# Performance work log

Hardware: AMD Instinct MI355X
Metric: run time of the kernel (lower is better)

Reference implementation:

```python
import jax, jax.numpy as jnp
import numpy as np

D = 128; H = 8; L = 3; FF = 512; HID = 512
B = 512; N = 20
KD = D // H
CLIP = 10.0


def _bn(x, g, b):
    # BatchNorm1d over flattened (B*n, D), training-mode batch stats, affine
    m = jnp.mean(x, axis=(0, 1)); v = jnp.var(x, axis=(0, 1))
    return (x - m) * jax.lax.rsqrt(v + 1e-5) * g + b


def _mha(x, Wq, Wk, Wv, Wo):
    q = jnp.einsum('bnd,hdk->hbnk', x, Wq)
    k = jnp.einsum('bnd,hdk->hbnk', x, Wk)
    v = jnp.einsum('bnd,hdk->hbnk', x, Wv)
    a = jax.nn.softmax(jnp.einsum('hbnk,hbmk->hbnm', q, k) / np.float32(np.sqrt(KD)), axis=-1)
    h = jnp.einsum('hbnm,hbmk->hbnk', a, v)
    return jnp.einsum('hbnk,hkd->bnd', h, Wo)


def _encode(x, Wq, Wk, Wv, Wo, g1, b1, fW1, fb1, fW2, fb2, g2, b2):
    for l in range(L):
        x = _bn(x + _mha(x, Wq[l], Wk[l], Wv[l], Wo[l]), g1[l], b1[l])
        f = jnp.maximum(x @ fW1[l] + fb1[l], 0.0) @ fW2[l] + fb2[l]
        x = _bn(x + f, g2[l], b2[l])
    return x


def _forward(coords, Wi, bi, W_ph, enc_Wq, enc_Wk, enc_Wv, enc_Wo, enc_g1, enc_b1,
             enc_ffW1, enc_ffb1, enc_ffW2, enc_ffb2, enc_g2, enc_b2,
             W_node, W_fixed, W_step, W_out, Wc1, bc1, Wc2, bc2):
    Bs, Ns, _ = coords.shape
    bid = jnp.arange(Bs)
    x = coords @ Wi + bi                                   # (B,N,D) initial embeddings
    crd = coords
    node_idx = jnp.broadcast_to(jnp.arange(Ns)[None, :], (Bs, Ns))
    # state is re-made each step, so step context is always the placeholder
    step_ctx = jnp.broadcast_to(W_ph[None, :], (Bs, 2 * D))
    ctx_q = step_ctx @ W_step                              # (B,D), constant across steps
    log_ps = []; irs = []; vals = []; tours = []
    first = prev = cur = None
    for i in range(Ns):  # sequential decode loop (shapes shrink each step)
        n = Ns - i
        E = _encode(x, enc_Wq, enc_Wk, enc_Wv, enc_Wo, enc_g1, enc_b1,
                    enc_ffW1, enc_ffb1, enc_ffW2, enc_ffb2, enc_g2, enc_b2)  # (B,n,D)
        g_mean = jnp.mean(E, axis=1)                       # (B,D)
        q = g_mean @ W_fixed + ctx_q                       # (B,D)
        gK, gV, lK = jnp.split(E @ W_node, 3, axis=-1)     # each (B,n,D)
        qh = q.reshape(Bs, H, KD)
        a = jax.nn.softmax(jnp.einsum('bhk,bnhk->bhn', qh, gK.reshape(Bs, n, H, KD)) / np.float32(np.sqrt(KD)), axis=-1)
        glimpse = jnp.einsum('bhn,bnhk->bhk', a, gV.reshape(Bs, n, H, KD)).reshape(Bs, D) @ W_out
        logits = jnp.tanh(jnp.einsum('bd,bnd->bn', glimpse, lK) / np.float32(np.sqrt(D))) * CLIP
        log_p = jax.nn.log_softmax(logits, axis=-1)        # mask all-False (fresh state)
        sel = jnp.argmax(log_p, axis=1)                    # greedy decode
        log_ps.append(log_p[bid, sel])
        cur = crd[bid, sel]
        if i == 0:
            first = cur
            irs.append(jnp.zeros((Bs,), coords.dtype))
        else:
            irs.append(-jnp.sqrt(jnp.sum((cur - prev) ** 2, axis=1)))
        h = jnp.maximum(jnp.concatenate([g_mean, step_ctx], axis=1) @ Wc1 + bc1, 0.0)
        vals.append((h @ Wc2 + bc2)[:, 0])
        tours.append(node_idx[bid, sel])
        if i < Ns - 1:
            sel_mask = (jnp.arange(n)[None, :] == sel[:, None]).astype(jnp.int32)
            keep = jnp.argsort(sel_mask, axis=1)[:, : n - 1]  # stable: drops selected, keeps order
            crd = jnp.take_along_axis(crd, keep[:, :, None], axis=1)
            x = jnp.take_along_axis(x, keep[:, :, None], axis=1)
            node_idx = jnp.take_along_axis(node_idx, keep, axis=1)
        prev = cur
    reward_final = -jnp.sqrt(jnp.sum((first - cur) ** 2, axis=1))
    tours = jnp.stack(tours, axis=1)                        # (B,N) int
    d = jnp.take_along_axis(coords, tours[:, :, None], axis=1)
    cost = jnp.sum(jnp.linalg.norm(d[:, 1:] - d[:, :-1], axis=2), axis=1) + jnp.linalg.norm(d[:, 0] - d[:, -1], axis=1)
    return (jnp.stack(log_ps, 1), jnp.stack(irs, 1), jnp.stack(vals, 1), cost, reward_final, tours)


def setup_inputs():
    key = jax.random.key(0)
    ks = jax.random.split(key, 16)
    def nrm(k, shp, scale=0.02):
        return jax.random.normal(k, shp, dtype=jnp.float32) * scale
    return {
        'coords': jax.random.uniform(ks[0], (B, N, 2), dtype=jnp.float32),
        'Wi': nrm(ks[1], (2, D), 0.5),
        'bi': jnp.zeros((D,), jnp.float32),
        'W_ph': jax.random.uniform(ks[2], (2 * D,), jnp.float32, -1.0, 1.0),
        'enc_Wq': nrm(ks[3], (L, H, D, KD)),
        'enc_Wk': nrm(ks[4], (L, H, D, KD)),
        'enc_Wv': nrm(ks[5], (L, H, D, KD)),
        'enc_Wo': nrm(ks[6], (L, H, KD, D)),
        'enc_g1': jnp.ones((L, D), jnp.float32),
        'enc_b1': jnp.zeros((L, D), jnp.float32),
        'enc_ffW1': nrm(ks[7], (L, D, FF)),
        'enc_ffb1': jnp.zeros((L, FF), jnp.float32),
        'enc_ffW2': nrm(ks[8], (L, FF, D)),
        'enc_ffb2': jnp.zeros((L, D), jnp.float32),
        'enc_g2': jnp.ones((L, D), jnp.float32),
        'enc_b2': jnp.zeros((L, D), jnp.float32),
        'W_node': nrm(ks[9], (D, 3 * D)),
        'W_fixed': nrm(ks[10], (D, D)),
        'W_step': nrm(ks[11], (2 * D, D)),
        'W_out': nrm(ks[12], (D, D)),
        'Wc1': nrm(ks[13], (3 * D, HID)),
        'bc1': jnp.zeros((HID,), jnp.float32),
        'Wc2': nrm(ks[14], (HID, 1)),
        'bc2': jnp.zeros((1,), jnp.float32),
    }


def reference(coords, Wi, bi, W_ph, enc_Wq, enc_Wk, enc_Wv, enc_Wo, enc_g1, enc_b1,
              enc_ffW1, enc_ffb1, enc_ffW2, enc_ffb2, enc_g2, enc_b2,
              W_node, W_fixed, W_step, W_out, Wc1, bc1, Wc2, bc2):
    return _forward(coords, Wi, bi, W_ph, enc_Wq, enc_Wk, enc_Wv, enc_Wo, enc_g1, enc_b1,
                    enc_ffW1, enc_ffb1, enc_ffW2, enc_ffb2, enc_g2, enc_b2,
                    W_node, W_fixed, W_step, W_out, Wc1, bc1, Wc2, bc2)
```

## Files before the change

### kernel.cpp

```cpp
#include <hip/hip_runtime.h>
#include <cmath>

namespace {
constexpr int Hc = 8, FFc = 512, HIDc = 512;
}

struct Params {
  const float *coords, *Wi, *bi, *W_ph;
  const float *Wq, *Wk, *Wv, *Wo, *g1, *b1, *fW1, *fb1, *fW2, *fb2, *g2, *b2;
  const float *W_node, *W_fixed, *W_step, *W_out, *Wc1, *bc1, *Wc2, *bc2;
  float* out;
};

__device__ __align__(16) float g_bn[120 * 8 * 256];
__device__ __align__(16) float g_x[512 * 2560];
__device__ __align__(16) float g_t[512 * 2560];
__device__ __align__(16) float g_h[512 * 2560];
__device__ __align__(16) float g_dec[512 * 7680];
__device__ __align__(16) float g_qv[512 * 128];
__device__ float g_val[512];
__device__ __align__(16) float g_crd[512 * 40];
__device__ int   g_idx[512 * 20];
__device__ float g_state[512 * 8];
__device__ __align__(16) float g_ctxq[128];
__device__ __align__(16) float g_cctx[512];
__device__ __align__(16) float g_Wqp[3 * 16384];
__device__ __align__(16) float g_Wkp[3 * 16384];
__device__ __align__(16) float g_Wvp[3 * 16384];
__device__ __align__(16) float g_Wop[3 * 16384];
__device__ __align__(16) float g_W1q[3 * 65536];
__device__ __align__(16) float g_W2q[3 * 65536];
__device__ __align__(16) float g_Wnp[49152];
__device__ __align__(16) float g_Wfp[16384];
__device__ __align__(16) float g_Woup[16384];
__device__ __align__(16) float g_Wc1p[65536];

#define DOT4(a, b) ((a).x*(b).x + (a).y*(b).y + (a).z*(b).z + (a).w*(b).w)

__device__ __forceinline__ void bn_coef(int slot, const float* g, const float* bb, float cnt,
                                        float* s_scale, float* s_shift, int tid) {
  if (tid < 128) {
    float sm = 0.f, sq = 0.f;
#pragma unroll
    for (int r = 0; r < 8; r++) {
      const float* s = &g_bn[(slot * 8 + r) * 256];
      sm += s[tid]; sq += s[128 + tid];
    }
    float m_ = sm / cnt;
    float v_ = sq / cnt - m_ * m_;
    float rs = rsqrtf(v_ + 1e-5f);
    float sc = rs * g[tid];
    s_scale[tid] = sc;
    s_shift[tid] = bb[tid] - m_ * sc;
  }
}

__global__ __launch_bounds__(256) void kinit(Params p) {
  const int tid = threadIdx.x, b = blockIdx.x;
  const int gid = b * 256 + tid, GS = 512 * 256;
  for (int i = gid; i < 120 * 8 * 256; i += GS) g_bn[i] = 0.f;
  if (gid < 512) g_val[gid] = 0.f;
  for (int e = tid; e < 2560; e += 256) {
    int i = e >> 7, d = e & 127;
    float cx = p.coords[b * 40 + 2 * i], cy = p.coords[b * 40 + 2 * i + 1];
    g_x[b * 2560 + e] = cx * p.Wi[d] + cy * p.Wi[128 + d] + p.bi[d];
  }
  if (tid < 40) g_crd[b * 40 + tid] = p.coords[b * 40 + tid];
  if (tid < 20) g_idx[b * 20 + tid] = tid;
  if (tid < 8) g_state[b * 8 + tid] = 0.f;
  if (b == 0) {
    if (tid < 128) {
      float a = 0.f;
      for (int j = 0; j < 256; j++) a += p.W_ph[j] * p.W_step[j * 128 + tid];
      g_ctxq[tid] = a;
    }
    for (int jj = tid; jj < 512; jj += 256) {
      float a = p.bc1[jj];
      for (int e = 0; e < 256; e++) a += p.W_ph[e] * p.Wc1[(128 + e) * 512 + jj];
      g_cctx[jj] = a;
    }
  }
  for (int e = gid; e < 3 * 16384; e += GS) {
    int sub = e & 3, rest = e >> 2;
    int j = rest & 127, rest2 = rest >> 7, d4 = rest2 & 31, l = rest2 >> 5;
    int d = d4 * 4 + sub;
    int src = l * 16384 + (j >> 4) * 2048 + d * 16 + (j & 15);
    g_Wqp[e] = p.Wq[src]; g_Wkp[e] = p.Wk[src]; g_Wvp[e] = p.Wv[src];
    int c = d;
    g_Wop[e] = p.Wo[l * 16384 + (c >> 4) * 2048 + (c & 15) * 128 + j];
  }
  for (int e = gid; e < 3 * 65536; e += GS) {
    int sub = e & 3, f = (e >> 2) & 16383, l = e >> 16;
    int cg = f & 63, c = (f >> 6) & 7, k4 = f >> 9;
    g_W1q[e] = p.fW1[l * 65536 + (k4 * 4 + sub) * 512 + cg * 8 + c];
  }
  for (int e = gid; e < 3 * 65536; e += GS) {
    int sub = e & 3, f = (e >> 2) & 16383, l = e >> 16;
    int cg = f & 31, c = (f >> 5) & 3, k4 = f >> 7;
    g_W2q[e] = p.fW2[l * 65536 + (k4 * 4 + sub) * 128 + cg * 4 + c];
  }
  for (int e = gid; e < 49152; e += GS) {
    int sub = e & 3, rest = e >> 2;
    int col = rest % 384, e4 = rest / 384;
    g_Wnp[e] = p.W_node[(e4 * 4 + sub) * 384 + col];
  }
  for (int e = gid; e < 16384; e += GS) {
    int sub = e & 3, rest = e >> 2;
    int j = rest & 127, e4 = rest >> 7;
    g_Wfp[e] = p.W_fixed[(e4 * 4 + sub) * 128 + j];
    g_Woup[e] = p.W_out[(e4 * 4 + sub) * 128 + j];
  }
  for (int e = gid; e < 65536; e += GS) {
    int sub = e & 3, rest = e >> 2;
    int jj = rest & 511, e4 = rest >> 9;
    g_Wc1p[e] = p.Wc1[(e4 * 4 + sub) * 512 + jj];
  }
}

__global__ __launch_bounds__(256) void ka1(Params p, int step, int l) {
  const int tid = threadIdx.x, b = blockIdx.x, hb = blockIdx.y;
  const int n = 20 - step;
  const int jc = tid & 63, rg = tid >> 6;
  __shared__ __align__(16) float s_t[2560];
  __shared__ __align__(16) float s_q[1280];
  __shared__ float s_kT[1280];
  __shared__ __align__(16) float s_v[1280];
  __shared__ float s_att[1600];
  __shared__ __align__(16) float s_scale[128], s_shift[128];

  if (l > 0)
    bn_coef(step * 6 + (l - 1) * 2 + 1, p.g2 + (l - 1) * 128, p.b2 + (l - 1) * 128,
            (float)(512 * n), s_scale, s_shift, tid);
  __syncthreads();
  const float4* src4 = (const float4*)((l == 0 ? g_x : g_t) + b * 2560);
  float4* st4 = (float4*)s_t;
  for (int e4 = tid; e4 < n * 32; e4 += 256) {
    float4 x = src4[e4];
    if (l > 0) {
      float4 sc = ((const float4*)s_scale)[e4 & 31];
      float4 sh = ((const float4*)s_shift)[e4 & 31];
      x.x = x.x * sc.x + sh.x; x.y = x.y * sc.y + sh.y;
      x.z = x.z * sc.z + sh.z; x.w = x.w * sc.w + sh.w;
    }
    st4[e4] = x;
  }
  __syncthreads();
  {
    const int j = hb * 64 + jc;
    const float4* wq4 = (const float4*)g_Wqp + l * 4096 + j;
    const float4* wk4 = (const float4*)g_Wkp + l * 4096 + j;
    const float4* wv4 = (const float4*)g_Wvp + l * 4096 + j;
    float aq[5], ak[5], av[5];
#pragma unroll
    for (int r = 0; r < 5; r++) { aq[r] = 0.f; ak[r] = 0.f; av[r] = 0.f; }
    for (int d4 = 0; d4 < 32; d4++) {
      float4 wq = wq4[d4 * 128], wk = wk4[d4 * 128], wv = wv4[d4 * 128];
#pragma unroll
      for (int r = 0; r < 5; r++) {
        int i = rg + 4 * r;
        if (i < n) {
          float4 x = st4[i * 32 + d4];
          aq[r] += DOT4(x, wq); ak[r] += DOT4(x, wk); av[r] += DOT4(x, wv);
        }
      }
    }
#pragma unroll
    for (int r = 0; r < 5; r++) {
      int i = rg + 4 * r;
      if (i < n) {
        s_q[i * 64 + jc] = aq[r];
        s_kT[jc * 20 + i] = ak[r];
        s_v[i * 64 + jc] = av[r];
      }
    }
  }
  __syncthreads();
  const int nn = n * n;
  for (int e = tid; e < 4 * nn; e += 256) {
    int hl = e / nn, rem = e % nn, i = rem / n, m = rem % n;
    float dacc = 0.f;
#pragma unroll
    for (int k2 = 0; k2 < 16; k2++)
      dacc += s_q[i * 64 + hl * 16 + k2] * s_kT[(hl * 16 + k2) * 20 + m];
    s_att[hl * 400 + i * 20 + m] = dacc * 0.25f;
  }
  __syncthreads();
  for (int r = tid; r < 4 * n; r += 256) {
    int hl = r / n, i = r % n;
    float* row = s_att + hl * 400 + i * 20;
    float mx = row[0];
    for (int m = 1; m < n; m++) mx = fmaxf(mx, row[m]);
    float s = 0.f;
    for (int m = 0; m < n; m++) { float ev = __expf(row[m] - mx); row[m] = ev; s += ev; }
    float inv = 1.f / s;
    for (int m = 0; m < n; m++) row[m] *= inv;
  }
  __syncthreads();
  for (int e = tid; e < 4 * n * 16; e += 256) {
    int hl = e / (n * 16), rem = e % (n * 16), i = rem >> 4, k2 = rem & 15;
    const float* arow = s_att + hl * 400 + i * 20;
    float acc = 0.f;
    for (int m = 0; m < n; m++) acc += arow[m] * s_v[m * 64 + hl * 16 + k2];
    g_h[b * 2560 + i * 128 + hb * 64 + hl * 16 + k2] = acc;
  }
}

__global__ __launch_bounds__(256) void ka2(Params p, int step, int l) {
  const int tid = threadIdx.x, b = blockIdx.x, s = blockIdx.y;
  const int n = 20 - step;
  const int jcol = tid & 127, rhalf = tid >> 7;
  __shared__ __align__(16) float s_h[2560];
  __shared__ __align__(16) float s_x[2560];
  __shared__ __align__(16) float s_scale[128], s_shift[128];
  __shared__ float s_sm[128], s_sq[128];

  if (l > 0)
    bn_coef(step * 6 + (l - 1) * 2 + 1, p.g2 + (l - 1) * 128, p.b2 + (l - 1) * 128,
            (float)(512 * n), s_scale, s_shift, tid);
  __syncthreads();
  const float4* src4 = (const float4*)((l == 0 ? g_x : g_t) + b * 2560);
  const float4* gh4 = (const float4*)(g_h + b * 2560);
  float4* sh4 = (float4*)s_h;
  float4* sx4 = (float4*)s_x;
  for (int e4 = tid; e4 < n * 32; e4 += 256) {
    int i = e4 >> 5;
    if (((i ^ s) & 1) == 0) {
      sh4[e4] = gh4[e4];
      float4 x = src4[e4];
      if (l > 0) {
        float4 sc = ((const float4*)s_scale)[e4 & 31];
        float4 sf = ((const float4*)s_shift)[e4 & 31];
        x.x = x.x * sc.x + sf.x; x.y = x.y * sc.y + sf.y;
        x.z = x.z * sc.z + sf.z; x.w = x.w * sc.w + sf.w;
      }
      sx4[e4] = x;
    }
  }
  __syncthreads();
  float acc[5];
#pragma unroll
  for (int r = 0; r < 5; r++) {
    int i = s + 2 * (rhalf + 2 * r);
    acc[r] = (i < n) ? s_x[i * 128 + jcol] : 0.f;
  }
  const float4* wo4 = (const float4*)g_Wop + l * 4096 + jcol;
  for (int c4 = 0; c4 < 32; c4++) {
    float4 w = wo4[c4 * 128];
#pragma unroll
    for (int r = 0; r < 5; r++) {
      int i = s + 2 * (rhalf + 2 * r);
      if (i < n) { float4 h = sh4[i * 32 + c4]; acc[r] += DOT4(h, w); }
    }
  }
  float sm = 0.f, sq = 0.f;
#pragma unroll
  for (int r = 0; r < 5; r++) {
    int i = s + 2 * (rhalf + 2 * r);
    if (i < n) { g_t[b * 2560 + i * 128 + jcol] = acc[r]; sm += acc[r]; sq += acc[r] * acc[r]; }
  }
  __syncthreads();
  if (rhalf == 1) { s_sm[jcol] = sm; s_sq[jcol] = sq; }
  __syncthreads();
  if (rhalf == 0) {
    float* slot = &g_bn[((step * 6 + l * 2) * 8 + ((b * 2 + s) & 7)) * 256];
    atomicAdd(&slot[jcol], sm + s_sm[jcol]);
    atomicAdd(&slot[128 + jcol], sq + s_sq[jcol]);
  }
}

__global__ __launch_bounds__(256) void kff(Params p, int step, int l) {
  const int tid = threadIdx.x, bx = blockIdx.x;
  const int n = 20 - step;
  const int r0 = bx * 16;
  __shared__ __align__(16) float s_x[16 * 128];
  __shared__ __align__(16) float s_hid[16 * 512];
  __shared__ __align__(16) float s_scale[128], s_shift[128];
  __shared__ float s_bn[8 * 128 * 2];

  bn_coef(step * 6 + l * 2, p.g1 + l * 128, p.b1 + l * 128, (float)(512 * n), s_scale, s_shift, tid);
  __syncthreads();
  {
    float4* sx4 = (float4*)s_x;
    for (int e4 = tid; e4 < 16 * 32; e4 += 256) {
      int row = e4 >> 5, d4 = e4 & 31;
      int r = r0 + row, b = r / n, i = r - b * n;
      float4 x = *(const float4*)(g_t + b * 2560 + i * 128 + d4 * 4);
      float4 sc = ((const float4*)s_scale)[d4];
      float4 sf = ((const float4*)s_shift)[d4];
      x.x = x.x * sc.x + sf.x; x.y = x.y * sc.y + sf.y;
      x.z = x.z * sc.z + sf.z; x.w = x.w * sc.w + sf.w;
      sx4[e4] = x;
    }
  }
  __syncthreads();
  {
    const int cg = tid & 63, rg = tid >> 6;
    float acc[4][8];
#pragma unroll
    for (int rr = 0; rr < 4; rr++)
#pragma unroll
      for (int c = 0; c < 8; c++) acc[rr][c] = 0.f;
    const float4* w1 = (const float4*)g_W1q + l * 16384 + cg;
    const float4* xx = (const float4*)s_x + rg * 4 * 32;
    for (int k4 = 0; k4 < 32; k4++) {
      float4 xr0 = xx[k4], xr1 = xx[32 + k4], xr2 = xx[64 + k4], xr3 = xx[96 + k4];
#pragma unroll
      for (int c = 0; c < 8; c++) {
        float4 w = w1[(k4 * 8 + c) * 64];
        acc[0][c] += DOT4(xr0, w); acc[1][c] += DOT4(xr1, w);
        acc[2][c] += DOT4(xr2, w); acc[3][c] += DOT4(xr3, w);
      }
    }
    float4 b1a = *(const float4*)(p.fb1 + l * FFc + cg * 8);
    float4 b1b = *(const float4*)(p.fb1 + l * FFc + cg * 8 + 4);
#pragma unroll
    for (int rr = 0; rr < 4; rr++) {
      int row = rg * 4 + rr;
      float4 u0, u1;
      u0.x = fmaxf(acc[rr][0] + b1a.x, 0.f); u0.y = fmaxf(acc[rr][1] + b1a.y, 0.f);
      u0.z = fmaxf(acc[rr][2] + b1a.z, 0.f); u0.w = fmaxf(acc[rr][3] + b1a.w, 0.f);
      u1.x = fmaxf(acc[rr][4] + b1b.x, 0.f); u1.y = fmaxf(acc[rr][5] + b1b.y, 0.f);
      u1.z = fmaxf(acc[rr][6] + b1b.z, 0.f); u1.w = fmaxf(acc[rr][7] + b1b.w, 0.f);
      *(float4*)&s_hid[row * 512 + cg * 8] = u0;
      *(float4*)&s_hid[row * 512 + cg * 8 + 4] = u1;
    }
  }
  __syncthreads();
  {
    const int cg = tid & 31, rg = tid >> 5;
    float acc0[4], acc1[4];
#pragma unroll
    for (int c = 0; c < 4; c++) { acc0[c] = 0.f; acc1[c] = 0.f; }
    const float4* w2 = (const float4*)g_W2q + l * 16384 + cg;
    const float4* hh = (const float4*)s_hid + rg * 2 * 128;
    for (int k4 = 0; k4 < 128; k4++) {
      float4 h0 = hh[k4], h1 = hh[128 + k4];
#pragma unroll
      for (int c = 0; c < 4; c++) {
        float4 w = w2[(k4 * 4 + c) * 32];
        acc0[c] += DOT4(h0, w); acc1[c] += DOT4(h1, w);
      }
    }
    float4 f2 = *(const float4*)(p.fb2 + l * 128 + cg * 4);
#pragma unroll
    for (int rr = 0; rr < 2; rr++) {
      int row = rg * 2 + rr;
      int r = r0 + row, b = r / n, i = r - b * n;
      float4 xr = ((const float4*)s_x)[row * 32 + cg];
      float4 u;
      u.x = xr.x + (rr ? acc1[0] : acc0[0]) + f2.x;
      u.y = xr.y + (rr ? acc1[1] : acc0[1]) + f2.y;
      u.z = xr.z + (rr ? acc1[2] : acc0[2]) + f2.z;
      u.w = xr.w + (rr ? acc1[3] : acc0[3]) + f2.w;
      *(float4*)(g_t + b * 2560 + i * 128 + cg * 4) = u;
      if (rr == 0) {
        s_bn[(rg * 128 + cg * 4 + 0) * 2] = u.x; s_bn[(rg * 128 + cg * 4 + 0) * 2 + 1] = u.x * u.x;
        s_bn[(rg * 128 + cg * 4 + 1) * 2] = u.y; s_bn[(rg * 128 + cg * 4 + 1) * 2 + 1] = u.y * u.y;
        s_bn[(rg * 128 + cg * 4 + 2) * 2] = u.z; s_bn[(rg * 128 + cg * 4 + 2) * 2 + 1] = u.z * u.z;
        s_bn[(rg * 128 + cg * 4 + 3) * 2] = u.w; s_bn[(rg * 128 + cg * 4 + 3) * 2 + 1] = u.w * u.w;
      } else {
        s_bn[(rg * 128 + cg * 4 + 0) * 2] += u.x; s_bn[(rg * 128 + cg * 4 + 0) * 2 + 1] += u.x * u.x;
        s_bn[(rg * 128 + cg * 4 + 1) * 2] += u.y; s_bn[(rg * 128 + cg * 4 + 1) * 2 + 1] += u.y * u.y;
        s_bn[(rg * 128 + cg * 4 + 2) * 2] += u.z; s_bn[(rg * 128 + cg * 4 + 2) * 2 + 1] += u.z * u.z;
        s_bn[(rg * 128 + cg * 4 + 3) * 2] += u.w; s_bn[(rg * 128 + cg * 4 + 3) * 2 + 1] += u.w * u.w;
      }
    }
  }
  __syncthreads();
  if (tid < 128) {
    float sm = 0.f, sq = 0.f;
#pragma unroll
    for (int rg = 0; rg < 8; rg++) { sm += s_bn[(rg * 128 + tid) * 2]; sq += s_bn[(rg * 128 + tid) * 2 + 1]; }
    float* slot = &g_bn[((step * 6 + l * 2 + 1) * 8 + (bx & 7)) * 256];
    atomicAdd(&slot[tid], sm);
    atomicAdd(&slot[128 + tid], sq);
  }
}

__global__ __launch_bounds__(256) void kd1(Params p, int step) {
  const int tid = threadIdx.x, b = blockIdx.x, bc = blockIdx.y;
  const int n = 20 - step;
  const int cb = tid & 63, rg = tid >> 6;
  __shared__ __align__(16) float s_t[2560];
  __shared__ __align__(16) float s_scale[128], s_shift[128];
  __shared__ __align__(16) float s_gmean[128];
  __shared__ float s_red[256];

  bn_coef(step * 6 + 5, p.g2 + 2 * 128, p.b2 + 2 * 128, (float)(512 * n), s_scale, s_shift, tid);
  __syncthreads();
  const float4* src4 = (const float4*)(g_t + b * 2560);
  float4* st4 = (float4*)s_t;
  for (int e4 = tid; e4 < n * 32; e4 += 256) {
    float4 x = src4[e4];
    float4 sc = ((const float4*)s_scale)[e4 & 31];
    float4 sf = ((const float4*)s_shift)[e4 & 31];
    x.x = x.x * sc.x + sf.x; x.y = x.y * sc.y + sf.y;
    x.z = x.z * sc.z + sf.z; x.w = x.w * sc.w + sf.w;
    st4[e4] = x;
  }
  __syncthreads();
  if (tid < 128) {
    float ssum = 0.f;
    for (int i2 = 0; i2 < n; i2++) ssum += s_t[i2 * 128 + tid];
    s_gmean[tid] = ssum / (float)n;
  }
  __syncthreads();
  {
    float acc[3][5];
#pragma unroll
    for (int cc = 0; cc < 3; cc++)
#pragma unroll
      for (int r = 0; r < 5; r++) acc[cc][r] = 0.f;
    const float4* wn4 = (const float4*)g_Wnp + bc * 192 + cb;
    for (int d4 = 0; d4 < 32; d4++) {
      float4 w0 = wn4[d4 * 384], w1 = wn4[d4 * 384 + 64], w2 = wn4[d4 * 384 + 128];
#pragma unroll
      for (int r = 0; r < 5; r++) {
        int i = rg + 4 * r;
        if (i < n) {
          float4 x = st4[i * 32 + d4];
          acc[0][r] += DOT4(x, w0); acc[1][r] += DOT4(x, w1); acc[2][r] += DOT4(x, w2);
        }
      }
    }
#pragma unroll
// ... 117 lines not shown
  }
  __syncthreads();
  if (step < 19) {
    const int sel = s_sel;
    const int movecnt = (n - 1 - sel) * 128;
    float tmp[10]; float crdv = 0.f; int idxv = 0;
#pragma unroll
    for (int r = 0; r < 10; r++) { int e = tid + r * 256; if (e < movecnt) tmp[r] = g_x[b * 2560 + (sel + 1) * 128 + e]; }
    const int mc2 = (n - 1 - sel) * 2;
    if (tid < mc2) crdv = g_crd[b * 40 + (sel + 1) * 2 + tid];
    if (tid < n - 1 - sel) idxv = g_idx[b * 20 + sel + 1 + tid];
    __syncthreads();
#pragma unroll
    for (int r = 0; r < 10; r++) { int e = tid + r * 256; if (e < movecnt) g_x[b * 2560 + sel * 128 + e] = tmp[r]; }
    if (tid < mc2) g_crd[b * 40 + sel * 2 + tid] = crdv;
    if (tid < n - 1 - sel) g_idx[b * 20 + sel + tid] = idxv;
  }
}

extern "C" void kernel_launch(void* const* d_in, const int* in_sizes, int n_in,
                              void* d_out, int out_size, void* d_ws, size_t ws_size,
                              hipStream_t stream) {
  Params p;
  p.coords  = (const float*)d_in[0];
  p.Wi      = (const float*)d_in[1];
  p.bi      = (const float*)d_in[2];
  p.W_ph    = (const float*)d_in[3];
  p.Wq      = (const float*)d_in[4];
  p.Wk      = (const float*)d_in[5];
  p.Wv      = (const float*)d_in[6];
  p.Wo      = (const float*)d_in[7];
  p.g1      = (const float*)d_in[8];
  p.b1      = (const float*)d_in[9];
  p.fW1     = (const float*)d_in[10];
  p.fb1     = (const float*)d_in[11];
  p.fW2     = (const float*)d_in[12];
  p.fb2     = (const float*)d_in[13];
  p.g2      = (const float*)d_in[14];
  p.b2      = (const float*)d_in[15];
  p.W_node  = (const float*)d_in[16];
  p.W_fixed = (const float*)d_in[17];
  p.W_step  = (const float*)d_in[18];
  p.W_out   = (const float*)d_in[19];
  p.Wc1     = (const float*)d_in[20];
  p.bc1     = (const float*)d_in[21];
  p.Wc2     = (const float*)d_in[22];
  p.bc2     = (const float*)d_in[23];
  p.out = (float*)d_out;

  kinit<<<512, 256, 0, stream>>>(p);
  for (int step = 0; step < 20; step++) {
    const int n = 20 - step;
    for (int l = 0; l < 3; l++) {
      ka1<<<dim3(512, 2), 256, 0, stream>>>(p, step, l);
      ka2<<<dim3(512, 2), 256, 0, stream>>>(p, step, l);
      kff<<<dim3(32 * n), 256, 0, stream>>>(p, step, l);
    }
    kd1<<<dim3(512, 2), 256, 0, stream>>>(p, step);
    kd2<<<512, 256, 0, stream>>>(p, step);
  }
}
```

Before: 6.912 ms.

## Split attention into row-tiled QKV GEMM, per-batch attention, and row-tiled output projection

Replaces the per-batch fused attention kernel (which recomputed QKV projections per batch element with poor weight reuse) with a row-tiled QKV projection kernel over flattened B*n rows using a fused packed Wqkv layout, a separate per-batch attention kernel covering all 8 heads, and a row-tiled output-projection kernel with BN stat accumulation. The FF kernel tile shrinks from 16 to 8 rows per block to raise block count. This adds a kernel launch per layer and a global round trip for QKV (g_qkv), in exchange for better weight reuse and grid occupancy.

Result: slower. 9.614 ms (+39.1%).

```diff
diff --git a/kernel.cpp b/kernel.cpp
--- a/kernel.cpp
+++ b/kernel.cpp
@@ -16,6 +16,7 @@
 __device__ __align__(16) float g_x[512 * 2560];
 __device__ __align__(16) float g_t[512 * 2560];
 __device__ __align__(16) float g_h[512 * 2560];
+__device__ __align__(16) float g_qkv[512 * 7680];
 __device__ __align__(16) float g_dec[512 * 7680];
 __device__ __align__(16) float g_qv[512 * 128];
 __device__ float g_val[512];
@@ -24,10 +25,8 @@
 __device__ float g_state[512 * 8];
 __device__ __align__(16) float g_ctxq[128];
 __device__ __align__(16) float g_cctx[512];
-__device__ __align__(16) float g_Wqp[3 * 16384];
-__device__ __align__(16) float g_Wkp[3 * 16384];
-__device__ __align__(16) float g_Wvp[3 * 16384];
-__device__ __align__(16) float g_Wop[3 * 16384];
+__device__ __align__(16) float g_Wqkv[3 * 49152];
+__device__ __align__(16) float g_Wo2[3 * 16384];
 __device__ __align__(16) float g_W1q[3 * 65536];
 __device__ __align__(16) float g_W2q[3 * 65536];
 __device__ __align__(16) float g_Wnp[49152];
@@ -80,14 +79,21 @@
       g_cctx[jj] = a;
     }
   }
+  for (int e = gid; e < 3 * 49152; e += GS) {
+    int l = e / 49152, f = e % 49152;
+    int sub = f & 3, lane = (f >> 2) & 63, rest = f >> 8;
+    int c = rest % 6, k4 = rest / 6;
+    int col = c * 64 + lane, d = k4 * 4 + sub;
+    float v;
+    if (col < 128)      v = p.Wq[l * 16384 + (col >> 4) * 2048 + d * 16 + (col & 15)];
+    else if (col < 256) { int j = col - 128; v = p.Wk[l * 16384 + (j >> 4) * 2048 + d * 16 + (j & 15)]; }
+    else                { int j = col - 256; v = p.Wv[l * 16384 + (j >> 4) * 2048 + d * 16 + (j & 15)]; }
+    g_Wqkv[e] = v;
+  }
   for (int e = gid; e < 3 * 16384; e += GS) {
-    int sub = e & 3, rest = e >> 2;
-    int j = rest & 127, rest2 = rest >> 7, d4 = rest2 & 31, l = rest2 >> 5;
-    int d = d4 * 4 + sub;
-    int src = l * 16384 + (j >> 4) * 2048 + d * 16 + (j & 15);
-    g_Wqp[e] = p.Wq[src]; g_Wkp[e] = p.Wk[src]; g_Wvp[e] = p.Wv[src];
-    int c = d;
-    g_Wop[e] = p.Wo[l * 16384 + (c >> 4) * 2048 + (c & 15) * 128 + j];
+    int sub = e & 3, cg = (e >> 2) & 31, c = (e >> 7) & 3, k4 = (e >> 9) & 31, l = e >> 14;
+    int r = k4 * 4 + sub, j = c * 32 + cg;
+    g_Wo2[e] = p.Wo[l * 16384 + (r >> 4) * 2048 + (r & 15) * 128 + j];
   }
   for (int e = gid; e < 3 * 65536; e += GS) {
     int sub = e & 3, f = (e >> 2) & 16383, l = e >> 16;
@@ -117,77 +123,90 @@
   }
 }
 
-__global__ __launch_bounds__(256) void ka1(Params p, int step, int l) {
-  const int tid = threadIdx.x, b = blockIdx.x, hb = blockIdx.y;
+__global__ __launch_bounds__(256) void kqkv(Params p, int step, int l) {
+  const int tid = threadIdx.x, bx = blockIdx.x;
   const int n = 20 - step;
-  const int jc = tid & 63, rg = tid >> 6;
-  __shared__ __align__(16) float s_t[2560];
-  __shared__ __align__(16) float s_q[1280];
-  __shared__ float s_kT[1280];
-  __shared__ __align__(16) float s_v[1280];
-  __shared__ float s_att[1600];
+  const int r0 = bx * 8;
+  __shared__ __align__(16) float s_x[8 * 128];
   __shared__ __align__(16) float s_scale[128], s_shift[128];
 
   if (l > 0)
     bn_coef(step * 6 + (l - 1) * 2 + 1, p.g2 + (l - 1) * 128, p.b2 + (l - 1) * 128,
             (float)(512 * n), s_scale, s_shift, tid);
   __syncthreads();
-  const float4* src4 = (const float4*)((l == 0 ? g_x : g_t) + b * 2560);
-  float4* st4 = (float4*)s_t;
-  for (int e4 = tid; e4 < n * 32; e4 += 256) {
-    float4 x = src4[e4];
-    if (l > 0) {
-      float4 sc = ((const float4*)s_scale)[e4 & 31];
-      float4 sh = ((const float4*)s_shift)[e4 & 31];
-      x.x = x.x * sc.x + sh.x; x.y = x.y * sc.y + sh.y;
-      x.z = x.z * sc.z + sh.z; x.w = x.w * sc.w + sh.w;
-    }
-    st4[e4] = x;
-  }
-  __syncthreads();
-  {
-    const int j = hb * 64 + jc;
-    const float4* wq4 = (const float4*)g_Wqp + l * 4096 + j;
-    const float4* wk4 = (const float4*)g_Wkp + l * 4096 + j;
-    const float4* wv4 = (const float4*)g_Wvp + l * 4096 + j;
-    float aq[5], ak[5], av[5];
-#pragma unroll
-    for (int r = 0; r < 5; r++) { aq[r] = 0.f; ak[r] = 0.f; av[r] = 0.f; }
-    for (int d4 = 0; d4 < 32; d4++) {
-      float4 wq = wq4[d4 * 128], wk = wk4[d4 * 128], wv = wv4[d4 * 128];
-#pragma unroll
-      for (int r = 0; r < 5; r++) {
-        int i = rg + 4 * r;
-        if (i < n) {
-          float4 x = st4[i * 32 + d4];
-          aq[r] += DOT4(x, wq); ak[r] += DOT4(x, wk); av[r] += DOT4(x, wv);
-        }
+  {
+    const float* src = (l == 0) ? g_x : g_t;
+    float4* sx4 = (float4*)s_x;
+    for (int e4 = tid; e4 < 8 * 32; e4 += 256) {
+      int row = e4 >> 5, d4 = e4 & 31;
+      int r = r0 + row, b = r / n, i = r - b * n;
+      float4 x = *(const float4*)(src + b * 2560 + i * 128 + d4 * 4);
+      if (l > 0) {
+        float4 sc = ((const float4*)s_scale)[d4];
+        float4 sf = ((const float4*)s_shift)[d4];
+        x.x = x.x * sc.x + sf.x; x.y = x.y * sc.y + sf.y;
+        x.z = x.z * sc.z + sf.z; x.w = x.w * sc.w + sf.w;
       }
-    }
-#pragma unroll
-    for (int r = 0; r < 5; r++) {
-      int i = rg + 4 * r;
-      if (i < n) {
-        s_q[i * 64 + jc] = aq[r];
-        s_kT[jc * 20 + i] = ak[r];
-        s_v[i * 64 + jc] = av[r];
-      }
-    }
+      sx4[e4] = x;
+    }
+  }
+  __syncthreads();
+  const int lane = tid & 63, rg = tid >> 6;
+  float acc[2][6];
+#pragma unroll
+  for (int rr = 0; rr < 2; rr++)
+#pragma unroll
+    for (int c = 0; c < 6; c++) acc[rr][c] = 0.f;
+  const float4* wq = (const float4*)g_Wqkv + l * 12288 + lane;
+  const float4* xx = (const float4*)s_x + rg * 64;
+  for (int k4 = 0; k4 < 32; k4++) {
+    float4 x0 = xx[k4], x1 = xx[32 + k4];
+#pragma unroll
+    for (int c = 0; c < 6; c++) {
+      float4 w = wq[(k4 * 6 + c) * 64];
+      acc[0][c] += DOT4(x0, w); acc[1][c] += DOT4(x1, w);
+    }
+  }
+#pragma unroll
+  for (int rr = 0; rr < 2; rr++) {
+    int row = rg * 2 + rr;
+    int r = r0 + row, b = r / n, i = r - b * n;
+#pragma unroll
+    for (int c = 0; c < 6; c++)
+      g_qkv[b * 7680 + i * 384 + c * 64 + lane] = acc[rr][c];
+  }
+}
+
+__global__ __launch_bounds__(256) void katt(Params p, int step) {
+  const int tid = threadIdx.x, b = blockIdx.x;
+  const int n = 20 - step;
+  __shared__ __align__(16) float s_q[20 * 128];
+  __shared__ float s_kT[128 * 20];
+  __shared__ __align__(16) float s_v[20 * 128];
+  __shared__ float s_att[8 * 400];
+
+  for (int e = tid; e < n * 384; e += 256) {
+    int i = e / 384, c = e % 384;
+    float v = g_qkv[b * 7680 + e];
+    if (c < 128) s_q[i * 128 + c];
+    if (c < 128) s_q[i * 128 + c] = v;
+    else if (c < 256) s_kT[(c - 128) * 20 + i] = v;
+    else s_v[i * 128 + (c - 256)] = v;
   }
   __syncthreads();
   const int nn = n * n;
-  for (int e = tid; e < 4 * nn; e += 256) {
-    int hl = e / nn, rem = e % nn, i = rem / n, m = rem % n;
+  for (int e = tid; e < 8 * nn; e += 256) {
+    int hh = e / nn, rem = e % nn, i = rem / n, m = rem % n;
     float dacc = 0.f;
 #pragma unroll
     for (int k2 = 0; k2 < 16; k2++)
-      dacc += s_q[i * 64 + hl * 16 + k2] * s_kT[(hl * 16 + k2) * 20 + m];
-    s_att[hl * 400 + i * 20 + m] = dacc * 0.25f;
-  }
-  __syncthreads();
-  for (int r = tid; r < 4 * n; r += 256) {
-    int hl = r / n, i = r % n;
-    float* row = s_att + hl * 400 + i * 20;
+      dacc += s_q[i * 128 + hh * 16 + k2] * s_kT[(hh * 16 + k2) * 20 + m];
+    s_att[hh * 400 + i * 20 + m] = dacc * 0.25f;
+  }
+  __syncthreads();
+  for (int r = tid; r < 8 * n; r += 256) {
+    int hh = r / n, i = r % n;
+    float* row = s_att + hh * 400 + i * 20;
     float mx = row[0];
     for (int m = 1; m < n; m++) mx = fmaxf(mx, row[m]);
     float s = 0.f;
@@ -196,40 +215,40 @@
     for (int m = 0; m < n; m++) row[m] *= inv;
   }
   __syncthreads();
-  for (int e = tid; e < 4 * n * 16; e += 256) {
-    int hl = e / (n * 16), rem = e % (n * 16), i = rem >> 4, k2 = rem & 15;
-    const float* arow = s_att + hl * 400 + i * 20;
+  for (int e = tid; e < 8 * n * 16; e += 256) {
+    int hh = e / (n * 16), rem = e % (n * 16), i = rem >> 4, k2 = rem & 15;
+    const float* arow = s_att + hh * 400 + i * 20;
     float acc = 0.f;
-    for (int m = 0; m < n; m++) acc += arow[m] * s_v[m * 64 + hl * 16 + k2];
-    g_h[b * 2560 + i * 128 + hb * 64 + hl * 16 + k2] = acc;
-  }
-}
-
-__global__ __launch_bounds__(256) void ka2(Params p, int step, int l) {
-  const int tid = threadIdx.x, b = blockIdx.x, s = blockIdx.y;
+    for (int m = 0; m < n; m++) acc += arow[m] * s_v[m * 128 + hh * 16 + k2];
+    g_h[b * 2560 + i * 128 + hh * 16 + k2] = acc;
+  }
+}
+
+__global__ __launch_bounds__(256) void kout(Params p, int step, int l) {
+  const int tid = threadIdx.x, bx = blockIdx.x;
   const int n = 20 - step;
-  const int jcol = tid & 127, rhalf = tid >> 7;
-  __shared__ __align__(16) float s_h[2560];
-  __shared__ __align__(16) float s_x[2560];
+  const int r0 = bx * 8;
+  __shared__ __align__(16) float s_h[8 * 128];
+  __shared__ __align__(16) float s_x[8 * 128];
   __shared__ __align__(16) float s_scale[128], s_shift[128];
-  __shared__ float s_sm[128], s_sq[128];
+  __shared__ float s_bn[8 * 128 * 2];
 
   if (l > 0)
     bn_coef(step * 6 + (l - 1) * 2 + 1, p.g2 + (l - 1) * 128, p.b2 + (l - 1) * 128,
             (float)(512 * n), s_scale, s_shift, tid);
   __syncthreads();
-  const float4* src4 = (const float4*)((l == 0 ? g_x : g_t) + b * 2560);
-  const float4* gh4 = (const float4*)(g_h + b * 2560);
-  float4* sh4 = (float4*)s_h;
-  float4* sx4 = (float4*)s_x;
-  for (int e4 = tid; e4 < n * 32; e4 += 256) {
-    int i = e4 >> 5;
-    if (((i ^ s) & 1) == 0) {
-      sh4[e4] = gh4[e4];
-      float4 x = src4[e4];
+  {
+    const float* src = (l == 0) ? g_x : g_t;
+    float4* sx4 = (float4*)s_x;
+    float4* sh4 = (float4*)s_h;
+    for (int e4 = tid; e4 < 8 * 32; e4 += 256) {
+      int row = e4 >> 5, d4 = e4 & 31;
+      int r = r0 + row, b = r / n, i = r - b * n;
+      sh4[e4] = *(const float4*)(g_h + b * 2560 + i * 128 + d4 * 4);
+      float4 x = *(const float4*)(src + b * 2560 + i * 128 + d4 * 4);
       if (l > 0) {
-        float4 sc = ((const float4*)s_scale)[e4 & 31];
-        float4 sf = ((const float4*)s_shift)[e4 & 31];
+        float4 sc = ((const float4*)s_scale)[d4];
+        float4 sf = ((const float4*)s_shift)[d4];
         x.x = x.x * sc.x + sf.x; x.y = x.y * sc.y + sf.y;
         x.z = x.z * sc.z + sf.z; x.w = x.w * sc.w + sf.w;
       }
@@ -237,43 +256,48 @@
     }
   }
   __syncthreads();
-  float acc[5];
-#pragma unroll
-  for (int r = 0; r < 5; r++) {
-    int i = s + 2 * (rhalf + 2 * r);
-    acc[r] = (i < n) ? s_x[i * 128 + jcol] : 0.f;
-  }
-  const float4* wo4 = (const float4*)g_Wop + l * 4096 + jcol;
-  for (int c4 = 0; c4 < 32; c4++) {
-    float4 w = wo4[c4 * 128];
-#pragma unroll
-    for (int r = 0; r < 5; r++) {
-      int i = s + 2 * (rhalf + 2 * r);
-      if (i < n) { float4 h = sh4[i * 32 + c4]; acc[r] += DOT4(h, w); }
-    }
-  }
-  float sm = 0.f, sq = 0.f;
-#pragma unroll
-  for (int r = 0; r < 5; r++) {
-    int i = s + 2 * (rhalf + 2 * r);
-    if (i < n) { g_t[b * 2560 + i * 128 + jcol] = acc[r]; sm += acc[r]; sq += acc[r] * acc[r]; }
-  }
-  __syncthreads();
-  if (rhalf == 1) { s_sm[jcol] = sm; s_sq[jcol] = sq; }
-  __syncthreads();
-  if (rhalf == 0) {
-    float* slot = &g_bn[((step * 6 + l * 2) * 8 + ((b * 2 + s) & 7)) * 256];
-    atomicAdd(&slot[jcol], sm + s_sm[jcol]);
-    atomicAdd(&slot[128 + jcol], sq + s_sq[jcol]);
+  const int cg = tid & 31, rg = tid >> 5;
+  float acc[4];
+#pragma unroll
+  for (int c = 0; c < 4; c++) acc[c] = 0.f;
+  const float4* wo = (const float4*)g_Wo2 + l * 4096 + cg;
+  const float4* hh = (const float4*)s_h + rg * 32;
+  for (int k4 = 0; k4 < 32; k4++) {
+    float4 h = hh[k4];
+#pragma unroll
+    for (int c = 0; c < 4; c++) {
+      float4 w = wo[(k4 * 4 + c) * 32];
+      acc[c] += DOT4(h, w);
+    }
+  }
+  {
+    int r = r0 + rg, b = r / n, i = r - b * n;
+#pragma unroll
+    for (int c = 0; c < 4; c++) {
+      int col = c * 32 + cg;
+      float u = s_x[rg * 128 + col] + acc[c];
+      g_t[b * 2560 + i * 128 + col] = u;
+      s_bn[(rg * 128 + col) * 2] = u;
+      s_bn[(rg * 128 + col) * 2 + 1] = u * u;
+    }
+  }
+  __syncthreads();
+  if (tid < 128) {
+    float sm = 0.f, sq = 0.f;
+#pragma unroll
+    for (int rr = 0; rr < 8; rr++) { sm += s_bn[(rr * 128 + tid) * 2]; sq += s_bn[(rr * 128 + tid) * 2 + 1]; }
+    float* slot = &g_bn[((step * 6 + l * 2) * 8 + (bx & 7)) * 256];
+    atomicAdd(&slot[tid], sm);
+    atomicAdd(&slot[128 + tid], sq);
   }
 }
 
 __global__ __launch_bounds__(256) void kff(Params p, int step, int l) {
   const int tid = threadIdx.x, bx = blockIdx.x;
   const int n = 20 - step;
-  const int r0 = bx * 16;
-  __shared__ __align__(16) float s_x[16 * 128];
-  __shared__ __align__(16) float s_hid[16 * 512];
+  const int r0 = bx * 8;
+  __shared__ __align__(16) float s_x[8 * 128];
+  __shared__ __align__(16) float s_hid[8 * 512];
   __shared__ __align__(16) float s_scale[128], s_shift[128];
   __shared__ float s_bn[8 * 128 * 2];
 
@@ -281,7 +305,7 @@
   __syncthreads();
   {
     float4* sx4 = (float4*)s_x;
-    for (int e4 = tid; e4 < 16 * 32; e4 += 256) {
+    for (int e4 = tid; e4 < 8 * 32; e4 += 256) {
       int row = e4 >> 5, d4 = e4 & 31;
       int r = r0 + row, b = r / n, i = r - b * n;
       float4 x = *(const float4*)(g_t + b * 2560 + i * 128 + d4 * 4);
@@ -295,27 +319,26 @@
   __syncthreads();
   {
     const int cg = tid & 63, rg = tid >> 6;
-    float acc[4][8];
-#pragma unroll
-    for (int rr = 0; rr < 4; rr++)
+    float acc[2][8];
+#pragma unroll
+    for (int rr = 0; rr < 2; rr++)
 #pragma unroll
       for (int c = 0; c < 8; c++) acc[rr][c] = 0.f;
     const float4* w1 = (const float4*)g_W1q + l * 16384 + cg;
-    const float4* xx = (const float4*)s_x + rg * 4 * 32;
+    const float4* xx = (const float4*)s_x + rg * 64;
     for (int k4 = 0; k4 < 32; k4++) {
-      float4 xr0 = xx[k4], xr1 = xx[32 + k4], xr2 = xx[64 + k4], xr3 = xx[96 + k4];
+      float4 x0 = xx[k4], x1 = xx[32 + k4];
 #pragma unroll
       for (int c = 0; c < 8; c++) {
         float4 w = w1[(k4 * 8 + c) * 64];
-        acc[0][c] += DOT4(xr0, w); acc[1][c] += DOT4(xr1, w);
-        acc[2][c] += DOT4(xr2, w); acc[3][c] += DOT4(xr3, w);
+        acc[0][c] += DOT4(x0, w); acc[1][c] += DOT4(x1, w);
       }
     }
     float4 b1a = *(const float4*)(p.fb1 + l * FFc + cg * 8);
     float4 b1b = *(const float4*)(p.fb1 + l * FFc + cg * 8 + 4);
 #pragma unroll
-    for (int rr = 0; rr < 4; rr++) {
-      int row = rg * 4 + rr;
+    for (int rr = 0; rr < 2; rr++) {
+      int row = rg * 2 + rr;
       float4 u0, u1;
       u0.x = fmaxf(acc[rr][0] + b1a.x, 0.f); u0.y = fmaxf(acc[rr][1] + b1a.y, 0.f);
       u0.z = fmaxf(acc[rr][2] + b1a.z, 0.f); u0.w = fmaxf(acc[rr][3] + b1a.w, 0.f);
@@ -328,49 +351,38 @@
   __syncthreads();
   {
     const int cg = tid & 31, rg = tid >> 5;
-    float acc0[4], acc1[4];
-#pragma unroll
-    for (int c = 0; c < 4; c++) { acc0[c] = 0.f; acc1[c] = 0.f; }
+    float acc[4];
+#pragma unroll
+    for (int c = 0; c < 4; c++) acc[c] = 0.f;
     const float4* w2 = (const float4*)g_W2q + l * 16384 + cg;
-    const float4* hh = (const float4*)s_hid + rg * 2 * 128;
+    const float4* hh = (const float4*)s_hid + rg * 128;
     for (int k4 = 0; k4 < 128; k4++) {
-      float4 h0 = hh[k4], h1 = hh[128 + k4];
+      float4 h = hh[k4];
 #pragma unroll
       for (int c = 0; c < 4; c++) {
         float4 w = w2[(k4 * 4 + c) * 32];
-        acc0[c] += DOT4(h0, w); acc1[c] += DOT4(h1, w);
+        acc[c] += DOT4(h, w);
       }
     }
     float4 f2 = *(const float4*)(p.fb2 + l * 128 + cg * 4);
-#pragma unroll
-    for (int rr = 0; rr < 2; rr++) {
-      int row = rg * 2 + rr;
-      int r = r0 + row, b = r / n, i = r - b * n;
-      float4 xr = ((const float4*)s_x)[row * 32 + cg];
-      float4 u;
-      u.x = xr.x + (rr ? acc1[0] : acc0[0]) + f2.x;
-      u.y = xr.y + (rr ? acc1[1] : acc0[1]) + f2.y;
-      u.z = xr.z + (rr ? acc1[2] : acc0[2]) + f2.z;
-      u.w = xr.w + (rr ? acc1[3] : acc0[3]) + f2.w;
-      *(float4*)(g_t + b * 2560 + i * 128 + cg * 4) = u;
-      if (rr == 0) {
-        s_bn[(rg * 128 + cg * 4 + 0) * 2] = u.x; s_bn[(rg * 128 + cg * 4 + 0) * 2 + 1] = u.x * u.x;
-        s_bn[(rg * 128 + cg * 4 + 1) * 2] = u.y; s_bn[(rg * 128 + cg * 4 + 1) * 2 + 1] = u.y * u.y;
-        s_bn[(rg * 128 + cg * 4 + 2) * 2] = u.z; s_bn[(rg * 128 + cg * 4 + 2) * 2 + 1] = u.z * u.z;
-        s_bn[(rg * 128 + cg * 4 + 3) * 2] = u.w; s_bn[(rg * 128 + cg * 4 + 3) * 2 + 1] = u.w * u.w;
-      } else {
-        s_bn[(rg * 128 + cg * 4 + 0) * 2] += u.x; s_bn[(rg * 128 + cg * 4 + 0) * 2 + 1] += u.x * u.x;
-        s_bn[(rg * 128 + cg * 4 + 1) * 2] += u.y; s_bn[(rg * 128 + cg * 4 + 1) * 2 + 1] += u.y * u.y;
-        s_bn[(rg * 128 + cg * 4 + 2) * 2] += u.z; s_bn[(rg * 128 + cg * 4 + 2) * 2 + 1] += u.z * u.z;
-        s_bn[(rg * 128 + cg * 4 + 3) * 2] += u.w; s_bn[(rg * 128 + cg * 4 + 3) * 2 + 1] += u.w * u.w;
-      }
-    }
+    int r = r0 + rg, b = r / n, i = r - b * n;
+    float4 xr = ((const float4*)s_x)[rg * 32 + cg];
+    float4 u;
+    u.x = xr.x + acc[0] + f2.x;
+    u.y = xr.y + acc[1] + f2.y;
+    u.z = xr.z + acc[2] + f2.z;
+    u.w = xr.w + acc[3] + f2.w;
+    *(float4*)(g_t + b * 2560 + i * 128 + cg * 4) = u;
+    s_bn[(rg * 128 + cg * 4 + 0) * 2] = u.x; s_bn[(rg * 128 + cg * 4 + 0) * 2 + 1] = u.x * u.x;
+    s_bn[(rg * 128 + cg * 4 + 1) * 2] = u.y; s_bn[(rg * 128 + cg * 4 + 1) * 2 + 1] = u.y * u.y;
+    s_bn[(rg * 128 + cg * 4 + 2) * 2] = u.z; s_bn[(rg * 128 + cg * 4 + 2) * 2 + 1] = u.z * u.z;
+    s_bn[(rg * 128 + cg * 4 + 3) * 2] = u.w; s_bn[(rg * 128 + cg * 4 + 3) * 2 + 1] = u.w * u.w;
   }
   __syncthreads();
   if (tid < 128) {
     float sm = 0.f, sq = 0.f;
 #pragma unroll
-    for (int rg = 0; rg < 8; rg++) { sm += s_bn[(rg * 128 + tid) * 2]; sq += s_bn[(rg * 128 + tid) * 2 + 1]; }
+    for (int rr = 0; rr < 8; rr++) { sm += s_bn[(rr * 128 + tid) * 2]; sq += s_bn[(rr * 128 + tid) * 2 + 1]; }
     float* slot = &g_bn[((step * 6 + l * 2 + 1) * 8 + (bx & 7)) * 256];
     atomicAdd(&slot[tid], sm);
     atomicAdd(&slot[128 + tid], sq);
@@ -594,9 +606,10 @@
   for (int step = 0; step < 20; step++) {
     const int n = 20 - step;
     for (int l = 0; l < 3; l++) {
-      ka1<<<dim3(512, 2), 256, 0, stream>>>(p, step, l);
-      ka2<<<dim3(512, 2), 256, 0, stream>>>(p, step, l);
-      kff<<<dim3(32 * n), 256, 0, stream>>>(p, step, l);
+      kqkv<<<64 * n, 256, 0, stream>>>(p, step, l);
+      katt<<<512, 256, 0, stream>>>(p, step);
+      kout<<<64 * n, 256, 0, stream>>>(p, step, l);
+      kff<<<64 * n, 256, 0, stream>>>(p, step, l);
     }
     kd1<<<dim3(512, 2), 256, 0, stream>>>(p, step);
     kd2<<<512, 256, 0, stream>>>(p, step);
```

## Fuse attention and output projection into one per-batch kernel

Applied to the files above, without the earlier changes.

Merges the two attention kernels (QKV+softmax+AV, then Wo projection with residual and BN stats) into a single kernel with one block per batch element covering all 8 heads. The head output stays in shared memory instead of round-tripping through a global buffer, which removes one launch per layer and the extra global traffic. Q/K/V weights are packed into one interleaved buffer so each thread computes Q or K for all rows and half of V. In exchange each launch has half as many blocks, shared memory use roughly doubles and register pressure rises, which can lower occupancy.

Measured after the change: 8.184 ms. 18.4% more time.

```diff
diff --git a/kernel.cpp b/kernel.cpp
--- a/kernel.cpp
+++ b/kernel.cpp
@@ -15,7 +15,6 @@
 __device__ __align__(16) float g_bn[120 * 8 * 256];
 __device__ __align__(16) float g_x[512 * 2560];
 __device__ __align__(16) float g_t[512 * 2560];
-__device__ __align__(16) float g_h[512 * 2560];
 __device__ __align__(16) float g_dec[512 * 7680];
 __device__ __align__(16) float g_qv[512 * 128];
 __device__ float g_val[512];
@@ -24,9 +23,7 @@
 __device__ float g_state[512 * 8];
 __device__ __align__(16) float g_ctxq[128];
 __device__ __align__(16) float g_cctx[512];
-__device__ __align__(16) float g_Wqp[3 * 16384];
-__device__ __align__(16) float g_Wkp[3 * 16384];
-__device__ __align__(16) float g_Wvp[3 * 16384];
+__device__ __align__(16) float g_Wqkvp[3 * 49152];
 __device__ __align__(16) float g_Wop[3 * 16384];
 __device__ __align__(16) float g_W1q[3 * 65536];
 __device__ __align__(16) float g_W2q[3 * 65536];
@@ -80,13 +77,20 @@
       g_cctx[jj] = a;
     }
   }
+  for (int e = gid; e < 3 * 49152; e += GS) {
+    int sub = e & 3, q = e >> 2;
+    int col = q % 384, q2 = q / 384, d4 = q2 & 31, l = q2 >> 5;
+    int d = d4 * 4 + sub;
+    float v;
+    if (col < 128)      v = p.Wq[l * 16384 + (col >> 4) * 2048 + d * 16 + (col & 15)];
+    else if (col < 256) { int j = col - 128; v = p.Wk[l * 16384 + (j >> 4) * 2048 + d * 16 + (j & 15)]; }
+    else                { int j = col - 256; v = p.Wv[l * 16384 + (j >> 4) * 2048 + d * 16 + (j & 15)]; }
+    g_Wqkvp[e] = v;
+  }
   for (int e = gid; e < 3 * 16384; e += GS) {
     int sub = e & 3, rest = e >> 2;
-    int j = rest & 127, rest2 = rest >> 7, d4 = rest2 & 31, l = rest2 >> 5;
-    int d = d4 * 4 + sub;
-    int src = l * 16384 + (j >> 4) * 2048 + d * 16 + (j & 15);
-    g_Wqp[e] = p.Wq[src]; g_Wkp[e] = p.Wk[src]; g_Wvp[e] = p.Wv[src];
-    int c = d;
+    int j = rest & 127, rest2 = rest >> 7, c4 = rest2 & 31, l = rest2 >> 5;
+    int c = c4 * 4 + sub;
     g_Wop[e] = p.Wo[l * 16384 + (c >> 4) * 2048 + (c & 15) * 128 + j];
   }
   for (int e = gid; e < 3 * 65536; e += GS) {
@@ -117,23 +121,23 @@
   }
 }
 
-__global__ __launch_bounds__(256) void ka1(Params p, int step, int l) {
-  const int tid = threadIdx.x, b = blockIdx.x, hb = blockIdx.y;
+__global__ __launch_bounds__(256) void ka(Params p, int step, int l) {
+  const int tid = threadIdx.x, b = blockIdx.x;
   const int n = 20 - step;
-  const int jc = tid & 63, rg = tid >> 6;
-  __shared__ __align__(16) float s_t[2560];
-  __shared__ __align__(16) float s_q[1280];
-  __shared__ float s_kT[1280];
-  __shared__ __align__(16) float s_v[1280];
-  __shared__ float s_att[1600];
+  __shared__ __align__(16) float s_x[2560];
+  __shared__ __align__(16) float s_q[2560];
+  __shared__ float s_kT[2560];
+  __shared__ __align__(16) float s_v[2560];
+  __shared__ float s_att[3200];
   __shared__ __align__(16) float s_scale[128], s_shift[128];
+  __shared__ float s_sm[128], s_sq[128];
 
   if (l > 0)
     bn_coef(step * 6 + (l - 1) * 2 + 1, p.g2 + (l - 1) * 128, p.b2 + (l - 1) * 128,
             (float)(512 * n), s_scale, s_shift, tid);
   __syncthreads();
   const float4* src4 = (const float4*)((l == 0 ? g_x : g_t) + b * 2560);
-  float4* st4 = (float4*)s_t;
+  float4* st4 = (float4*)s_x;
   for (int e4 = tid; e4 < n * 32; e4 += 256) {
     float4 x = src4[e4];
     if (l > 0) {
@@ -146,48 +150,52 @@
   }
   __syncthreads();
   {
-    const int j = hb * 64 + jc;
-    const float4* wq4 = (const float4*)g_Wqp + l * 4096 + j;
-    const float4* wk4 = (const float4*)g_Wkp + l * 4096 + j;
-    const float4* wv4 = (const float4*)g_Wvp + l * 4096 + j;
-    float aq[5], ak[5], av[5];
-#pragma unroll
-    for (int r = 0; r < 5; r++) { aq[r] = 0.f; ak[r] = 0.f; av[r] = 0.f; }
-    for (int d4 = 0; d4 < 32; d4++) {
-      float4 wq = wq4[d4 * 128], wk = wk4[d4 * 128], wv = wv4[d4 * 128];
-#pragma unroll
-      for (int r = 0; r < 5; r++) {
-        int i = rg + 4 * r;
-        if (i < n) {
-          float4 x = st4[i * 32 + d4];
-          aq[r] += DOT4(x, wq); ak[r] += DOT4(x, wk); av[r] += DOT4(x, wv);
-        }
-      }
-    }
-#pragma unroll
-    for (int r = 0; r < 5; r++) {
-      int i = rg + 4 * r;
-      if (i < n) {
-        s_q[i * 64 + jc] = aq[r];
-        s_kT[jc * 20 + i] = ak[r];
-        s_v[i * 64 + jc] = av[r];
-      }
+    const int ph = tid >> 7, cB = tid & 127;
+    float a1[20], a2[10];
+#pragma unroll
+    for (int i = 0; i < 20; i++) a1[i] = 0.f;
+#pragma unroll
+    for (int r = 0; r < 10; r++) a2[r] = 0.f;
+    const float4* wp = (const float4*)g_Wqkvp + l * 12288;
+    for (int k4 = 0; k4 < 32; k4++) {
+      float4 wA = wp[k4 * 384 + tid];
+      float4 wB = wp[k4 * 384 + 256 + cB];
+#pragma unroll
+      for (int i = 0; i < 20; i++)
+        if (i < n) a1[i] += DOT4(st4[i * 32 + k4], wA);
+#pragma unroll
+      for (int r = 0; r < 10; r++) {
+        int i = 2 * r + ph;
+        if (i < n) a2[r] += DOT4(st4[i * 32 + k4], wB);
+      }
+    }
+    if (tid < 128) {
+#pragma unroll
+      for (int i = 0; i < 20; i++) if (i < n) s_q[i * 128 + tid] = a1[i];
+    } else {
+#pragma unroll
+      for (int i = 0; i < 20; i++) if (i < n) s_kT[(tid - 128) * 20 + i] = a1[i];
+    }
+#pragma unroll
+    for (int r = 0; r < 10; r++) {
+      int i = 2 * r + ph;
+      if (i < n) s_v[i * 128 + cB] = a2[r];
     }
   }
   __syncthreads();
   const int nn = n * n;
-  for (int e = tid; e < 4 * nn; e += 256) {
-    int hl = e / nn, rem = e % nn, i = rem / n, m = rem % n;
+  for (int e = tid; e < 8 * nn; e += 256) {
+    int hh = e / nn, rem = e % nn, i = rem / n, m = rem % n;
     float dacc = 0.f;
 #pragma unroll
     for (int k2 = 0; k2 < 16; k2++)
-      dacc += s_q[i * 64 + hl * 16 + k2] * s_kT[(hl * 16 + k2) * 20 + m];
-    s_att[hl * 400 + i * 20 + m] = dacc * 0.25f;
-  }
-  __syncthreads();
-  for (int r = tid; r < 4 * n; r += 256) {
-    int hl = r / n, i = r % n;
-    float* row = s_att + hl * 400 + i * 20;
+      dacc += s_q[i * 128 + hh * 16 + k2] * s_kT[(hh * 16 + k2) * 20 + m];
+    s_att[hh * 400 + i * 20 + m] = dacc * 0.25f;
+  }
+  __syncthreads();
+  for (int r = tid; r < 8 * n; r += 256) {
+    int hh = r / n, i = r % n;
+    float* row = s_att + hh * 400 + i * 20;
     float mx = row[0];
     for (int m = 1; m < n; m++) mx = fmaxf(mx, row[m]);
     float s = 0.f;
@@ -196,75 +204,46 @@
     for (int m = 0; m < n; m++) row[m] *= inv;
   }
   __syncthreads();
-  for (int e = tid; e < 4 * n * 16; e += 256) {
-    int hl = e / (n * 16), rem = e % (n * 16), i = rem >> 4, k2 = rem & 15;
-    const float* arow = s_att + hl * 400 + i * 20;
+  for (int e = tid; e < 8 * n * 16; e += 256) {
+    int hh = e / (n * 16), rem = e % (n * 16), i = rem >> 4, k2 = rem & 15;
+    const float* arow = s_att + hh * 400 + i * 20;
     float acc = 0.f;
-    for (int m = 0; m < n; m++) acc += arow[m] * s_v[m * 64 + hl * 16 + k2];
-    g_h[b * 2560 + i * 128 + hb * 64 + hl * 16 + k2] = acc;
-  }
-}
-
-__global__ __launch_bounds__(256) void ka2(Params p, int step, int l) {
-  const int tid = threadIdx.x, b = blockIdx.x, s = blockIdx.y;
-  const int n = 20 - step;
-  const int jcol = tid & 127, rhalf = tid >> 7;
-  __shared__ __align__(16) float s_h[2560];
-  __shared__ __align__(16) float s_x[2560];
-  __shared__ __align__(16) float s_scale[128], s_shift[128];
-  __shared__ float s_sm[128], s_sq[128];
-
-  if (l > 0)
-    bn_coef(step * 6 + (l - 1) * 2 + 1, p.g2 + (l - 1) * 128, p.b2 + (l - 1) * 128,
-            (float)(512 * n), s_scale, s_shift, tid);
-  __syncthreads();
-  const float4* src4 = (const float4*)((l == 0 ? g_x : g_t) + b * 2560);
-  const float4* gh4 = (const float4*)(g_h + b * 2560);
-  float4* sh4 = (float4*)s_h;
-  float4* sx4 = (float4*)s_x;
-  for (int e4 = tid; e4 < n * 32; e4 += 256) {
-    int i = e4 >> 5;
-    if (((i ^ s) & 1) == 0) {
-      sh4[e4] = gh4[e4];
-      float4 x = src4[e4];
-      if (l > 0) {
-        float4 sc = ((const float4*)s_scale)[e4 & 31];
-        float4 sf = ((const float4*)s_shift)[e4 & 31];
-        x.x = x.x * sc.x + sf.x; x.y = x.y * sc.y + sf.y;
-        x.z = x.z * sc.z + sf.z; x.w = x.w * sc.w + sf.w;
-      }
-      sx4[e4] = x;
-    }
-  }
-  __syncthreads();
-  float acc[5];
-#pragma unroll
-  for (int r = 0; r < 5; r++) {
-    int i = s + 2 * (rhalf + 2 * r);
-    acc[r] = (i < n) ? s_x[i * 128 + jcol] : 0.f;
-  }
-  const float4* wo4 = (const float4*)g_Wop + l * 4096 + jcol;
-  for (int c4 = 0; c4 < 32; c4++) {
-    float4 w = wo4[c4 * 128];
-#pragma unroll
-    for (int r = 0; r < 5; r++) {
-      int i = s + 2 * (rhalf + 2 * r);
-      if (i < n) { float4 h = sh4[i * 32 + c4]; acc[r] += DOT4(h, w); }
-    }
-  }
-  float sm = 0.f, sq = 0.f;
-#pragma unroll
-  for (int r = 0; r < 5; r++) {
-    int i = s + 2 * (rhalf + 2 * r);
-    if (i < n) { g_t[b * 2560 + i * 128 + jcol] = acc[r]; sm += acc[r]; sq += acc[r] * acc[r]; }
-  }
-  __syncthreads();
-  if (rhalf == 1) { s_sm[jcol] = sm; s_sq[jcol] = sq; }
-  __syncthreads();
-  if (rhalf == 0) {
-    float* slot = &g_bn[((step * 6 + l * 2) * 8 + ((b * 2 + s) & 7)) * 256];
-    atomicAdd(&slot[jcol], sm + s_sm[jcol]);
-    atomicAdd(&slot[128 + jcol], sq + s_sq[jcol]);
+    for (int m = 0; m < n; m++) acc += arow[m] * s_v[m * 128 + hh * 16 + k2];
+    s_q[i * 128 + hh * 16 + k2] = acc;
+  }
+  __syncthreads();
+  {
+    const int jcol = tid & 127, rhalf = tid >> 7;
+    float acc[10];
+#pragma unroll
+    for (int r = 0; r < 10; r++) {
+      int i = rhalf + 2 * r;
+      acc[r] = (i < n) ? s_x[i * 128 + jcol] : 0.f;
+    }
+    const float4* wo4 = (const float4*)g_Wop + l * 4096 + jcol;
+    const float4* sh4 = (const float4*)s_q;
+    for (int c4 = 0; c4 < 32; c4++) {
+      float4 w = wo4[c4 * 128];
+#pragma unroll
+      for (int r = 0; r < 10; r++) {
+        int i = rhalf + 2 * r;
+        if (i < n) acc[r] += DOT4(sh4[i * 32 + c4], w);
+      }
+    }
+    float sm = 0.f, sq = 0.f;
+#pragma unroll
+    for (int r = 0; r < 10; r++) {
+      int i = rhalf + 2 * r;
+      if (i < n) { g_t[b * 2560 + i * 128 + jcol] = acc[r]; sm += acc[r]; sq += acc[r] * acc[r]; }
+    }
+    __syncthreads();
+    if (rhalf == 1) { s_sm[jcol] = sm; s_sq[jcol] = sq; }
+    __syncthreads();
+    if (rhalf == 0) {
+      float* slot = &g_bn[((step * 6 + l * 2) * 8 + (b & 7)) * 256];
+      atomicAdd(&slot[jcol], sm + s_sm[jcol]);
+      atomicAdd(&slot[128 + jcol], sq + s_sq[jcol]);
+    }
   }
 }
 
@@ -594,8 +573,7 @@
   for (int step = 0; step < 20; step++) {
     const int n = 20 - step;
     for (int l = 0; l < 3; l++) {
-      ka1<<<dim3(512, 2), 256, 0, stream>>>(p, step, l);
-      ka2<<<dim3(512, 2), 256, 0, stream>>>(p, step, l);
+      ka<<<512, 256, 0, stream>>>(p, step, l);
       kff<<<dim3(32 * n), 256, 0, stream>>>(p, step, l);
     }
     kd1<<<dim3(512, 2), 256, 0, stream>>>(p, step);
```
